# Performance work log

Hardware: AMD Instinct MI355X
Metric: run time of the kernel (lower is better)

## Reference

```python
import jax, jax.numpy as jnp
import numpy as np

B, S, T, H, E, V = 64, 128, 64, 512, 256, 10000


def setup_inputs() -> dict:
    key = jax.random.key(0)
    ks = jax.random.split(key, 16)
    w = 0.05
    return {
        "trg": jax.random.randint(ks[0], (B, T), 0, V),
        "encoder_hidden": jax.random.normal(ks[1], (B, S, 2 * H), jnp.float32),
        "src_lengths": jax.random.randint(ks[2], (B,), 1, S + 1),
        "h0": jax.random.normal(ks[3], (B, H), jnp.float32),
        "c0": jax.random.normal(ks[4], (B, H), jnp.float32),
        "emb_table": jax.random.normal(ks[5], (V, E), jnp.float32) * w,
        "Wkey": jax.random.normal(ks[6], (2 * H, H), jnp.float32) * w,      # attention.key_layer
        "Wquery": jax.random.normal(ks[7], (H, H), jnp.float32) * w,        # attention.query_layer
        "we": jax.random.normal(ks[8], (H,), jnp.float32) * w,              # attention.energy_layer
        "W_ih": jax.random.normal(ks[9], (4 * H, E + 2 * H), jnp.float32) * w,
        "W_hh": jax.random.normal(ks[10], (4 * H, H), jnp.float32) * w,
        "b_ih": jnp.zeros((4 * H,), jnp.float32),
        "b_hh": jnp.zeros((4 * H,), jnp.float32),
        "Wpre": jax.random.normal(ks[11], (3 * H + E, H), jnp.float32) * w,  # pre_output_layer (no bias)
        "Wgen": jax.random.normal(ks[12], (H, V), jnp.float32) * w,          # generator / softmax head
    }


def reference(trg, encoder_hidden, src_lengths, h0, c0, emb_table, Wkey, Wquery,
              we, W_ih, W_hh, b_ih, b_hh, Wpre, Wgen):
    # Teacher-forced unroll (teacher_forcing=True branch); dropout in eval mode.
    s = encoder_hidden.shape[1]
    proj_key = encoder_hidden @ Wkey                            # [B,S,H]
    mask = jnp.arange(s)[None, :] < src_lengths[:, None]        # [B,S]
    embs = emb_table[trg]                                       # [B,T,E]

    def step(carry, emb_t):
        h, c = carry                                            # [B,H] each
        q = h @ Wquery                                          # query = last-layer hidden
        e = jnp.einsum('bsh,h->bs', jnp.tanh(q[:, None, :] + proj_key), we)
        a = jax.nn.softmax(jnp.where(mask, e, -1e9), axis=-1)   # masked attention
        ctx = jnp.einsum('bs,bsd->bd', a, encoder_hidden)       # [B,2H]
        x = jnp.concatenate([emb_t, ctx], axis=-1)              # rnn_input
        g = x @ W_ih.T + h @ W_hh.T + b_ih + b_hh
        i_g, f_g, g_g, o_g = jnp.split(g, 4, axis=-1)           # torch LSTM gate order
        c_new = jax.nn.sigmoid(f_g) * c + jax.nn.sigmoid(i_g) * jnp.tanh(g_g)
        h_new = jax.nn.sigmoid(o_g) * jnp.tanh(c_new)
        pre = jnp.concatenate([emb_t, h_new, ctx], axis=-1) @ Wpre
        logp = jax.nn.log_softmax(pre @ Wgen, axis=-1)          # [B,V]
        return (h_new, c_new), logp

    (hf, cf), out = jax.lax.scan(step, (h0, c0), jnp.swapaxes(embs, 0, 1))
    return jnp.transpose(out, (1, 2, 0)), hf, cf                # out: [B,V,T]
```

## Files before the change

### kernel.cpp

```cpp
#include <hip/hip_runtime.h>

#define B 64
#define S 128
#define T 64
#define H 512
#define E 256
#define V 10000
#define H2 1024
#define G4 2048
#define KX 1536
#define KP 1792
#define VP 10112
#define NROW 4096

typedef unsigned short u16;
typedef __attribute__((ext_vector_type(8))) short bf16x8;
typedef __attribute__((ext_vector_type(4))) short bf16x4;
typedef __attribute__((ext_vector_type(4))) float floatx4;

__device__ inline float b2f(u16 h){
  union { unsigned int u; float f; } v; v.u = ((unsigned int)h) << 16; return v.f;
}
__device__ inline u16 f2b(float f){
  union { unsigned int u; float f; } v; v.f = f;
  unsigned int r = v.u + 0x7FFFu + ((v.u >> 16) & 1u);
  return (u16)(r >> 16);
}
__device__ __forceinline__ float rcpf(float x){ return __builtin_amdgcn_rcpf(x); }
__device__ inline float sigf(float x){ return rcpf(1.f + __expf(-x)); }
__device__ inline float tanh_fast(float x){ float e=__expf(2.f*x); return 1.f - 2.f*rcpf(e+1.f); }

__device__ __forceinline__ void st_wt_u32(u16* p, unsigned v){
  asm volatile("global_store_dword %0, %1, off sc0 sc1" :: "v"(p), "v"(v) : "memory");
}
__device__ __forceinline__ void st_wt_u16(u16* p, unsigned v){
  asm volatile("global_store_short %0, %1, off sc0 sc1" :: "v"(p), "v"(v) : "memory");
}
__device__ __forceinline__ unsigned ld_if(unsigned* p){
  unsigned v;
  asm volatile("global_load_dword %0, %1, off sc0 sc1\ns_waitcnt vmcnt(0)" : "=v"(v) : "v"(p) : "memory");
  return v;
}
__device__ __forceinline__ void st_if(unsigned* p, unsigned v){
  asm volatile("global_store_dword %0, %1, off sc0 sc1\ns_waitcnt vmcnt(0)" :: "v"(p), "v"(v) : "memory");
}

#define BAR_WORDS (128*64)

__global__ void k_cast(const float* __restrict__ src, u16* __restrict__ dst, int n){
  int i = blockIdx.x*256 + threadIdx.x;
  if (i < n) dst[i] = f2b(src[i]);
}
__global__ void k_tct(const float* __restrict__ src, u16* __restrict__ dst, int R, int C){
  __shared__ float tile[64][65];
  int c0 = blockIdx.x*64, r0 = blockIdx.y*64;
  int tid = threadIdx.x;
  #pragma unroll
  for (int i=0;i<16;i++){
    int flat = i*256 + tid;
    int rr = flat >> 6, cc = flat & 63;
    int c = c0 + cc;
    tile[rr][cc] = (c < C) ? src[(size_t)(r0+rr)*C + c] : 0.f;
  }
  __syncthreads();
  #pragma unroll
  for (int i=0;i<16;i++){
    int flat = i*256 + tid;
    int cc = flat >> 6, rr = flat & 63;
    dst[(size_t)(c0+cc)*R + r0 + rr] = f2b(tile[rr][cc]);
  }
}
__global__ void k_encT(const float* __restrict__ enc, u16* __restrict__ o){
  __shared__ float tile[64][65];
  int d0 = blockIdx.x*64, s0 = blockIdx.y*64, b = blockIdx.z;
  int tid = threadIdx.x;
  #pragma unroll
  for (int i=0;i<16;i++){
    int flat = i*256 + tid;
    int sl = flat >> 6, dl = flat & 63;
    tile[sl][dl] = enc[((size_t)(b*S) + s0+sl)*H2 + d0+dl];
  }
  __syncthreads();
  #pragma unroll
  for (int i=0;i<16;i++){
    int flat = i*256 + tid;
    int dl = flat >> 6, sl = flat & 63;
    o[((size_t)b*H2 + d0+dl)*S + s0+sl] = f2b(tile[sl][dl]);
  }
}
__global__ void k_wch(const float* __restrict__ wih, const float* __restrict__ whh, u16* __restrict__ o){
  int i = blockIdx.x*256 + threadIdx.x;
  if (i < G4*KX){
    int gp = i / KX, k = i % KX;
    int j = gp >> 2, gate = gp & 3, g = gate*H + j;
    float v = (k < H2) ? wih[(size_t)g*(E+H2) + E + k] : whh[(size_t)g*H + (k - H2)];
    o[i] = f2b(v);
  }
}
__global__ void k_wihe(const float* __restrict__ wih, u16* __restrict__ o){
  int i = blockIdx.x*256 + threadIdx.x;
  if (i < G4*E){
    int gp = i / E, e = i % E;
    int j = gp >> 2, gate = gp & 3, g = gate*H + j;
    o[i] = f2b(wih[(size_t)g*(E+H2) + e]);
  }
}
__global__ void k_bias(const float* __restrict__ bi, const float* __restrict__ bh, float* __restrict__ o){
  int i = blockIdx.x*256 + threadIdx.x;
  if (i < G4){
    int j = i >> 2, gate = i & 3, g = gate*H + j;
    o[i] = bi[g] + bh[g];
  }
}
__global__ void k_emb(const int* __restrict__ trg, const float* __restrict__ emb, u16* __restrict__ catp){
  int i = blockIdx.x*256 + threadIdx.x;
  if (i < NROW*E){
    int row = i >> 8, e = i & 255;
    int tok = trg[row];
    catp[(size_t)row*KP + e] = f2b(emb[(size_t)tok*E + e]);
  }
}
__global__ void k_init(const float* __restrict__ h0, u16* __restrict__ xgs){
  int i = blockIdx.x*256 + threadIdx.x;
  if (i < B*H){
    int b = i >> 9, j = i & 511;
    xgs[(size_t)b*KX + H2 + j] = f2b(h0[i]);
  }
}
__global__ void k_zero(unsigned* bar){
  int i = blockIdx.x*256 + threadIdx.x;
  if (i < BAR_WORDS) bar[i] = 0u;
}
__global__ void k_lse(const float* __restrict__ sep, float* __restrict__ lse){
  int r = blockIdx.x*256 + threadIdx.x;
  if (r < NROW){
    float s = 0.f;
    for (int i=0;i<79;i++) s += sep[(size_t)r*80 + i];
    lse[r] = logf(s);
  }
}

template<int TN, int EPI>
__global__ __launch_bounds__(256) void gemm_bf16(
    const u16* __restrict__ A, int lda,
    const u16* __restrict__ BT, int ldb,
    int K,
    u16* outb, int ldc,
    float* sep,
    float* outp, const float* lse)
{
  constexpr int NSUB = TN/16;
  constexpr int NB = TN/64;
  __shared__ u16 sA[64*32];
  __shared__ u16 sB[TN*32];
  __shared__ float Cx[(EPI==3) ? 128*65 : 1];
  __shared__ float lseb[(EPI==3)?64:1];

  const int tid = threadIdx.x;
  const int lane = tid & 63;
  const int wv = tid >> 6;
  const int row0 = blockIdx.x * 64;
  const int n0 = blockIdx.y * TN;

  floatx4 acc[NSUB];
  #pragma unroll
  for (int s=0;s<NSUB;s++) acc[s] = (floatx4){0.f,0.f,0.f,0.f};

  const int ar = tid >> 2;
  const int ch = tid & 3;
  const int swz = (ar >> 1) & 3;
  const int px = ((lane & 15) >> 1) & 3;

  const u16* gA = A + (size_t)(row0+ar)*lda + ch*8;
  bf16x8 pa = *(const bf16x8*)gA;
  bf16x8 pb[NB];
  #pragma unroll
  for (int i=0;i<NB;i++) pb[i] = *(const bf16x8*)(BT + (size_t)(n0+i*64+ar)*ldb + ch*8);

  for (int k0 = 0; k0 < K; k0 += 32){
    __syncthreads();
    *(bf16x8*)&sA[ar*32 + ((ch ^ swz)*8)] = pa;
    #pragma unroll
    for (int i=0;i<NB;i++)
      *(bf16x8*)&sB[(i*64+ar)*32 + ((ch ^ swz)*8)] = pb[i];
    __syncthreads();
    if (k0 + 32 < K){
      pa = *(const bf16x8*)(gA + k0 + 32);
      #pragma unroll
      for (int i=0;i<NB;i++) pb[i] = *(const bf16x8*)(BT + (size_t)(n0+i*64+ar)*ldb + k0+32 + ch*8);
    }
    bf16x8 af = *(const bf16x8*)&sA[(16*wv + (lane&15))*32 + (((lane>>4) ^ px)*8)];
    #pragma unroll
    for (int s=0;s<NSUB;s++){
      bf16x8 bfv = *(const bf16x8*)&sB[(16*s + (lane&15))*32 + (((lane>>4) ^ px)*8)];
      acc[s] = __builtin_amdgcn_mfma_f32_16x16x32_bf16(af, bfv, acc[s], 0, 0, 0);
    }
  }

  if constexpr (EPI == 0 || EPI == 4){
    #pragma unroll
    for (int s=0;s<NSUB;s++)
      #pragma unroll
      for (int r=0;r<4;r++){
        int row = row0 + 16*wv + ((lane>>4)<<2) + r;
        int col = n0 + 16*s + (lane&15);
        if (EPI == 4) row = ((row & 63) << 6) | (row >> 6);
        outb[(size_t)row*ldc + col] = f2b(acc[s][r]);
      }
  }
  if constexpr (EPI == 2){
    float sr[4] = {0.f,0.f,0.f,0.f};
    #pragma unroll
    for (int s=0;s<NSUB;s++){
      int col = n0 + 16*s + (lane&15);
      if (col < V){
        #pragma unroll
        for (int r=0;r<4;r++) sr[r] += __expf(acc[s][r]);
      }
    }
    #pragma unroll
    for (int r=0;r<4;r++){
      float v = sr[r];
      v += __shfl_xor(v,1); v += __shfl_xor(v,2); v += __shfl_xor(v,4); v += __shfl_xor(v,8);
      sr[r] = v;
    }
    if ((lane&15)==0){
      #pragma unroll
      for (int r=0;r<4;r++){
        int row = row0 + 16*wv + ((lane>>4)<<2) + r;
        sep[(size_t)row*80 + blockIdx.y] = sr[r];
      }
    }
  }
  if constexpr (EPI == 3){
    #pragma unroll
    for (int s=0;s<NSUB;s++)
      #pragma unroll
      for (int r=0;r<4;r++){
        int rl = 16*wv + ((lane>>4)<<2) + r;
        int cl = 16*s + (lane&15);
        Cx[cl*65 + rl] = acc[s][r];
      }
    if (tid < 64) lseb[tid] = lse[row0 + tid];
    __syncthreads();
    int b = blockIdx.x;
    for (int idx = tid; idx < TN*16; idx += 256){
      int vl = idx >> 4, q4 = idx & 15;
      int v = n0 + vl;
      if (v < V){
        floatx4 o;
        o[0] = Cx[vl*65 + q4*4+0] - lseb[q4*4+0];
        o[1] = Cx[vl*65 + q4*4+1] - lseb[q4*4+1];
        o[2] = Cx[vl*65 + q4*4+2] - lseb[q4*4+2];
        o[3] = Cx[vl*65 + q4*4+3] - lseb[q4*4+3];
        *(floatx4*)&outp[((size_t)b*V + v)*T + q4*4] = o;
      }
    }
  }
}

__device__ __forceinline__ void wait_flags(unsigned* base, unsigned g){
  if (threadIdx.x < 64){
    unsigned* p = base + (unsigned)threadIdx.x*64;
    if (ld_if(p) < g){
      int it = 0;
      do { asm volatile("s_sleep 8":::); } while (ld_if(p) < g && ++it < 1000000);
    }
  }
  __syncthreads();
}

__global__ __launch_bounds__(512) void decoder_loop(
    u16* __restrict__ xgs, const float* __restrict__ c0f, float* __restrict__ outp,
    const u16* __restrict__ pk, const u16* __restrict__ encbT,
    const float* __restrict__ we, const int* __restrict__ lens,
    const u16* __restrict__ wqT, u16* __restrict__ cph,
    const u16* __restrict__ wch, const u16* __restrict__ gembt,
    const float* __restrict__ bias, unsigned* __restrict__ bar)
{
  __shared__ char pool[140288];

  const int tid = threadIdx.x, lane = tid & 63, wv = tid >> 6;
  const int blk = blockIdx.x;
  const int xcd = blk & 7, slot = blk >> 3;
  unsigned* flag_ctx = bar;
  unsigned* flag_h   = bar + 64*64;

  if (slot < 8){
    u16*   hsb  = (u16*)pool;
    float* qw   = (float*)(pool + 1024);
    float* wel  = (float*)(pool + 3072);
    float* ep   = (float*)(pool + 5120);
    float* ev   = (float*)(pool + 7168);
    u16*   alb  = (u16*)(pool + 7680);
    float* ctxf = (float*)(pool + 8192);

    const int b = xcd*8 + slot;
    const int lenb = lens[b];
    const int nks = (lenb + 31) >> 5;
    wel[tid] = we[tid];
    __syncthreads();

    for (int t=0; t<T; t++){
      wait_flags(flag_h, (unsigned)t);
      u16* xgt = xgs + (size_t)t*B*KX;
      hsb[tid] = xgt[b*KX + H2 + tid];
      __syncthreads();
      {
        floatx4 accq[4];
        #pragma unroll
        for (int s=0;s<4;s++) accq[s] = (floatx4){0.f,0.f,0.f,0.f};
        const int kc = (lane>>4)*8;
        #pragma unroll 4
        for (int ks=0; ks<16; ks++){
          bf16x8 af = *(const bf16x8*)&hsb[ks*32 + kc];
          #pragma unroll
          for (int s=0;s<4;s++){
            const u16* bp = wqT + (size_t)(wv*64 + s*16 + (lane&15))*H + ks*32 + kc;
            accq[s] = __builtin_amdgcn_mfma_f32_16x16x32_bf16(af, *(const bf16x8*)bp, accq[s], 0, 0, 0);
          }
        }
        if (lane < 16){
          #pragma unroll
          for (int s=0;s<4;s++) qw[wv*64 + s*16 + lane] = accq[s][0];
        }
      }
      __syncthreads();
      {
        int s = tid >> 2, part = tid & 3;
        float a0 = 0.f;
        if (s < lenb){
          const u16* pr = pk + (size_t)(b*S + s)*H;
          #pragma unroll 4
          for (int m=0;m<16;m++){
            int k0 = part*8 + m*32;
            bf16x8 p8 = *(const bf16x8*)(pr + k0);
            floatx4 qa = *(const floatx4*)&qw[k0];
            floatx4 qb = *(const floatx4*)&qw[k0+4];
            floatx4 wa = *(const floatx4*)&wel[k0];
            floatx4 wb = *(const floatx4*)&wel[k0+4];
            #pragma unroll
            for (int i=0;i<4;i++){
              a0 += tanh_fast(qa[i] + b2f((u16)p8[i]))   * wa[i];
              a0 += tanh_fast(qb[i] + b2f((u16)p8[i+4])) * wb[i];
            }
          }
        }
        ep[tid] = a0;
      }
      __syncthreads();
      if (wv == 0){
        int s0 = lane, s1 = lane + 64;
        float e0 = ep[s0*4]+ep[s0*4+1]+ep[s0*4+2]+ep[s0*4+3];
        float e1 = ep[s1*4]+ep[s1*4+1]+ep[s1*4+2]+ep[s1*4+3];
        bool m0 = s0 < lenb, m1 = s1 < lenb;
        float mx = fmaxf(m0 ? e0 : -1e30f, m1 ? e1 : -1e30f);
        #pragma unroll
        for (int o=32;o>=1;o>>=1) mx = fmaxf(mx, __shfl_xor(mx,o));
        float p0 = m0 ? __expf(e0-mx) : 0.f;
        float p1 = m1 ? __expf(e1-mx) : 0.f;
        float sm = p0 + p1;
        #pragma unroll
        for (int o=32;o>=1;o>>=1) sm += __shfl_xor(sm,o);
        float sinv = rcpf(sm);
        alb[s0] = f2b(p0*sinv);
        alb[s1] = f2b(p1*sinv);
      }
      __syncthreads();
      {
        floatx4 accc[8];
        #pragma unroll
        for (int s=0;s<8;s++) accc[s] = (floatx4){0.f,0.f,0.f,0.f};
        const int kc = (lane>>4)*8;
        for (int ks=0; ks<nks; ks++){
          bf16x8 af = *(const bf16x8*)&alb[ks*32 + kc];
          #pragma unroll
          for (int s8=0;s8<8;s8++){
            const u16* bp = encbT + ((size_t)b*H2 + wv*128 + s8*16 + (lane&15))*S + ks*32 + kc;
            accc[s8] = __builtin_amdgcn_mfma_f32_16x16x32_bf16(af, *(const bf16x8*)bp, accc[s8], 0, 0, 0);
          }
        }
        if (lane < 16){
          #pragma unroll
          for (int s8=0;s8<8;s8++) ctxf[wv*128 + s8*16 + lane] = accc[s8][0];
        }
      }
      __syncthreads();
      {
        int d = tid*2;
        unsigned pack = ((unsigned)f2b(ctxf[d+1]) << 16) | (unsigned)f2b(ctxf[d]);
        st_wt_u32(xgt + (size_t)b*KX + d, pack);
        *(unsigned*)&cph[(size_t)(b*T + t)*KP + E + H + d] = pack;
      }
      asm volatile("s_waitcnt vmcnt(0)" ::: "memory");
      __syncthreads();
      if (tid == 0) st_if(flag_ctx + (unsigned)b*64, (unsigned)(t+1));
      __syncthreads();
    }
  } else {
    u16*   sB  = (u16*)pool;
    u16*   sA0 = (u16*)(pool + 98304);
    u16*   sA1 = (u16*)(pool + 114688);
    float* Cx  = (float*)(pool + 131072);

    const int g = slot - 8;
    const int gid = xcd*8 + g;
    const int n0 = xcd*256 + g*32;
    const int kh = wv >> 2, wr = wv & 3;
    const int rs0 = tid >> 4, gs = tid & 15;
    const int rowa = 16*wr + (lane & 15);
    const int pb_ = tid >> 3, jl = tid & 7;
    const int jglob = n0/4 + jl;
    float creg = c0f[pb_*H + jglob];
    floatx4 bias4 = *(const floatx4*)(bias + n0 + jl*4);

    for (int u = tid; u < 32*192; u += 512){
      int row = u / 192, cl = u % 192;
      int kk = cl >> 4, c = cl & 15;
      *(bf16x8*)&sB[row*1536 + kk*128 + ((c ^ (row&7))*8)] =
          *(const bf16x8*)(wch + (size_t)(n0+row)*KX + kk*128 + c*8);
    }
    __syncthreads();

    for (int t=0; t<T; t++){
      const u16* xgt = xgs + (size_t)t*B*KX;
      u16* xgn = xgs + (size_t)(t+1)*B*KX;
      bf16x4 g4 = *(const bf16x4*)(gembt + (size_t)(t*B + pb_)*G4 + n0 + jl*4);

      floatx4 gacc[2];
      gacc[0] = (floatx4){0.f,0.f,0.f,0.f};
      gacc[1] = (floatx4){0.f,0.f,0.f,0.f};

      {
        bf16x8 a0 = *(const bf16x8*)(xgt + (size_t)rs0*KX + 8*128 + gs*8);
        bf16x8 a1 = *(const bf16x8*)(xgt + (size_t)(rs0+32)*KX + 8*128 + gs*8);
        for (int kk=8; kk<12; kk++){
          u16* sAc = (kk & 1) ? sA1 : sA0;
          *(bf16x8*)&sAc[rs0*128 + ((gs ^ (rs0&7))*8)] = a0;
          *(bf16x8*)&sAc[(rs0+32)*128 + ((gs ^ (rs0&7))*8)] = a1;
          __syncthreads();
          if (kk < 11){
            int ko = (kk+1)*128;
            a0 = *(const bf16x8*)(xgt + (size_t)rs0*KX + ko + gs*8);
            a1 = *(const bf16x8*)(xgt + (size_t)(rs0+32)*KX + ko + gs*8);
          }
          #pragma unroll
          for (int ks=0; ks<2; ks++){
            int gq = kh*8 + ks*4 + (lane>>4);
            bf16x8 af = *(const bf16x8*)&sAc[rowa*128 + ((gq ^ (rowa&7))*8)];
            #pragma unroll
            for (int s=0;s<2;s++){
              int rowb = 16*s + (lane & 15);
              bf16x8 bfv = *(const bf16x8*)&sB[rowb*1536 + kk*128 + ((gq ^ (rowb&7))*8)];
              gacc[s] = __builtin_amdgcn_mfma_f32_16x16x32_bf16(af, bfv, gacc[s], 0, 0, 0);
            }
          }
          __syncthreads();
        }
      }
      wait_flags(flag_ctx, (unsigned)(t+1));
      {
        bf16x8 a0 = *(const bf16x8*)(xgt + (size_t)rs0*KX + gs*8);
        bf16x8 a1 = *(const bf16x8*)(xgt + (size_t)(rs0+32)*KX + gs*8);
        for (int kk=0; kk<8; kk++){
          u16* sAc = (kk & 1) ? sA1 : sA0;
          *(bf16x8*)&sAc[rs0*128 + ((gs ^ (rs0&7))*8)] = a0;
          *(bf16x8*)&sAc[(rs0+32)*128 + ((gs ^ (rs0&7))*8)] = a1;
          __syncthreads();
          if (kk < 7){
            int ko = (kk+1)*128;
            a0 = *(const bf16x8*)(xgt + (size_t)rs0*KX + ko + gs*8);
            a1 = *(const bf16x8*)(xgt + (size_t)(rs0+32)*KX + ko + gs*8);
          }
          #pragma unroll
          for (int ks=0; ks<2; ks++){
            int gq = kh*8 + ks*4 + (lane>>4);
            bf16x8 af = *(const bf16x8*)&sAc[rowa*128 + ((gq ^ (rowa&7))*8)];
            #pragma unroll
            for (int s=0;s<2;s++){
              int rowb = 16*s + (lane & 15);
              bf16x8 bfv = *(const bf16x8*)&sB[rowb*1536 + kk*128 + ((gq ^ (rowb&7))*8)];
              gacc[s] = __builtin_amdgcn_mfma_f32_16x16x32_bf16(af, bfv, gacc[s], 0, 0, 0);
            }
          }
          __syncthreads();
        }
      }
      {
        int r0 = 16*wr + ((lane>>4)<<2);
        if (kh == 1){
          #pragma unroll
          for (int s=0;s<2;s++)
            #pragma unroll
            for (int r=0;r<4;r++) Cx[(r0+r)*36 + 16*s + (lane&15)] = gacc[s][r];
        }
      }
      __syncthreads();
      {
        int r0 = 16*wr + ((lane>>4)<<2);
        if (kh == 0){
          #pragma unroll
          for (int s=0;s<2;s++)
            #pragma unroll
            for (int r=0;r<4;r++) Cx[(r0+r)*36 + 16*s + (lane&15)] += gacc[s][r];
        }
      }
      __syncthreads();
      {
        float gi = Cx[pb_*36 + jl*4+0] + b2f((u16)g4[0]) + bias4[0];
        float gf = Cx[pb_*36 + jl*4+1] + b2f((u16)g4[1]) + bias4[1];
        float gg = Cx[pb_*36 + jl*4+2] + b2f((u16)g4[2]) + bias4[2];
        float go = Cx[pb_*36 + jl*4+3] + b2f((u16)g4[3]) + bias4[3];
        float cn = sigf(gf)*creg + sigf(gi)*tanh_fast(gg);
        float hn = sigf(go)*tanh_fast(cn);
        creg = cn;
        u16 hb = f2b(hn);
        st_wt_u16(xgn + (size_t)pb_*KX + H2 + jglob, (unsigned)hb);
        cph[(size_t)(pb_*T + t)*KP + E + jglob] = hb;
        if (t == T-1){
          outp[(size_t)B*V*T + pb_*H + jglob] = hn;
          outp[(size_t)B*V*T + B*H + pb_*H + jglob] = cn;
        }
      }
      asm volatile("s_waitcnt vmcnt(0)" ::: "memory");
      __syncthreads();
      if (tid == 0) st_if(flag_h + (unsigned)gid*64, (unsigned)(t+1));
      __syncthreads();
    }
  }
}

static inline int cdiv(int a, int b){ return (a + b - 1) / b; }

extern "C" void kernel_launch(void* const* d_in, const int* in_sizes, int n_in,
                              void* d_out, int out_size, void* d_ws, size_t ws_size,
                              hipStream_t stream)
{
  (void)in_sizes; (void)n_in; (void)out_size; (void)ws_size;
  const int*   trg  = (const int*)d_in[0];
  const float* enc  = (const float*)d_in[1];
  const int*   lens = (const int*)d_in[2];
  const float* h0   = (const float*)d_in[3];
  const float* c0   = (const float*)d_in[4];
  const float* embt = (const float*)d_in[5];
  const float* wkey = (const float*)d_in[6];
  const float* wqry = (const float*)d_in[7];
  const float* we   = (const float*)d_in[8];
  const float* wih  = (const float*)d_in[9];
  const float* whh  = (const float*)d_in[10];
  const float* bi   = (const float*)d_in[11];
  const float* bh   = (const float*)d_in[12];
  const float* wpre = (const float*)d_in[13];
  const float* wgen = (const float*)d_in[14];
  float* out = (float*)d_out;

  char* p = (char*)d_ws;
  auto carve = [&](size_t bytes)->char*{ char* r = p; p += (bytes + 255) & ~(size_t)255; return r; };
  u16*   encb  = (u16*)  carve((size_t)B*S*H2*2);
  u16*   encbT = (u16*)  carve((size_t)B*H2*S*2);
  u16*   pkb   = (u16*)  carve((size_t)B*S*H*2);
  u16*   catp  = (u16*)  carve((size_t)NROW*KP*2);
  u16*   gembb = (u16*)  carve((size_t)NROW*G4*2);
  u16*   preb  = (u16*)  carve((size_t)NROW*H*2);
  u16*   wgt   = (u16*)  carve((size_t)VP*H*2);
  u16*   wch   = (u16*)  carve((size_t)G4*KX*2);
  u16*   wihe  = (u16*)  carve((size_t)G4*E*2);
  u16*   wkeyT = (u16*)  carve((size_t)H*H2*2);
  u16*   wqT   = (u16*)  carve((size_t)H*H*2);
  u16*   wpreT = (u16*)  carve((size_t)H*KP*2);
  u16*   xgs   = (u16*)  carve((size_t)(T+1)*B*KX*2);
  float* biasp = (float*)carve((size_t)G4*4);
  float* sep   = (float*)carve((size_t)NROW*80*4);
  float* lse   = (float*)carve((size_t)NROW*4);
  unsigned* bar = (unsigned*)carve(BAR_WORDS*4);

  k_cast<<<cdiv(B*S*H2,256),256,0,stream>>>(enc, encb, B*S*H2);
  k_encT<<<dim3(H2/64, S/64, B),256,0,stream>>>(enc, encbT);
  k_tct<<<dim3(H/64, H/64),256,0,stream>>>(wqry, wqT, H, H);
  k_tct<<<dim3(H/64, H2/64),256,0,stream>>>(wkey, wkeyT, H2, H);
  k_tct<<<dim3(H/64, KP/64),256,0,stream>>>(wpre, wpreT, KP, H);
  k_tct<<<dim3(VP/64, H/64),256,0,stream>>>(wgen, wgt, H, V);
  k_wch<<<cdiv(G4*KX,256),256,0,stream>>>(wih, whh, wch);
  k_wihe<<<cdiv(G4*E,256),256,0,stream>>>(wih, wihe);
  k_bias<<<cdiv(G4,256),256,0,stream>>>(bi, bh, biasp);
  k_emb<<<cdiv(NROW*E,256),256,0,stream>>>(trg, embt, catp);
  k_init<<<cdiv(B*H,256),256,0,stream>>>(h0, xgs);
  k_zero<<<cdiv(BAR_WORDS,256),256,0,stream>>>(bar);

  gemm_bf16<64,0><<<dim3(B*S/64, H/64),256,0,stream>>>(
      encb, H2, wkeyT, H2, H2, pkb, H, nullptr, nullptr, nullptr);
  gemm_bf16<64,4><<<dim3(NROW/64, G4/64),256,0,stream>>>(
      catp, KP, wihe, E, E, gembb, G4, nullptr, nullptr, nullptr);

  decoder_loop<<<128,512,0,stream>>>(xgs, c0, out, pkb, encbT, we, lens,
                                     wqT, catp, wch, gembb, biasp, bar);

  gemm_bf16<64,0><<<dim3(NROW/64, H/64),256,0,stream>>>(
      catp, KP, wpreT, KP, KP, preb, H, nullptr, nullptr, nullptr);

  gemm_bf16<128,2><<<dim3(NROW/64, VP/128),256,0,stream>>>(
      preb, H, wgt, H, H, nullptr, 0, sep, nullptr, nullptr);
  k_lse<<<cdiv(NROW,256),256,0,stream>>>(sep, lse);
  gemm_bf16<128,3><<<dim3(NROW/64, VP/128),256,0,stream>>>(
      preb, H, wgt, H, H, nullptr, 0, nullptr, out, lse);
}
```

Measured before the change: 2.516 ms.

## Repartition LSTM gate blocks by batch group to localize cross-block synchronization

Gate blocks now each own 8 batch rows and 64 hidden units (all four gates) instead of all 64 batch rows for 32 gate columns. Each block then waits on only 8 flags, the attention blocks for its batch group and the hidden-state producers it depends on, instead of all 64. Gate weights are no longer held in LDS; they are streamed from global memory with register prefetch, which cuts LDS use and removes the K-split reduction and the double-buffered A staging. Spin-wait sleep is also shortened. The cost is more weight traffic from global/L2 on every step, and MFMA tiles are half wasted because only 8 of 16 rows are used.

```diff
diff --git a/kernel.cpp b/kernel.cpp
--- a/kernel.cpp
+++ b/kernel.cpp
@@ -259,12 +259,12 @@
   }
 }
 
-__device__ __forceinline__ void wait_flags(unsigned* base, unsigned g){
-  if (threadIdx.x < 64){
-    unsigned* p = base + (unsigned)threadIdx.x*64;
+__device__ __forceinline__ void wait8(unsigned* bar, int base, int stride, unsigned g){
+  if (threadIdx.x < 8){
+    unsigned* p = bar + (unsigned)(base + (int)threadIdx.x*stride)*64;
     if (ld_if(p) < g){
       int it = 0;
-      do { asm volatile("s_sleep 8":::); } while (ld_if(p) < g && ++it < 1000000);
+      do { asm volatile("s_sleep 2":::); } while (ld_if(p) < g && ++it < 2000000);
     }
   }
   __syncthreads();
@@ -278,31 +278,29 @@
     const u16* __restrict__ wch, const u16* __restrict__ gembt,
     const float* __restrict__ bias, unsigned* __restrict__ bar)
 {
-  __shared__ char pool[140288];
+  __shared__ char pool[61440];
 
   const int tid = threadIdx.x, lane = tid & 63, wv = tid >> 6;
   const int blk = blockIdx.x;
   const int xcd = blk & 7, slot = blk >> 3;
-  unsigned* flag_ctx = bar;
-  unsigned* flag_h   = bar + 64*64;
 
   if (slot < 8){
     u16*   hsb  = (u16*)pool;
     float* qw   = (float*)(pool + 1024);
     float* wel  = (float*)(pool + 3072);
     float* ep   = (float*)(pool + 5120);
-    float* ev   = (float*)(pool + 7168);
     u16*   alb  = (u16*)(pool + 7680);
     float* ctxf = (float*)(pool + 8192);
 
     const int b = xcd*8 + slot;
+    const int x = xcd;
     const int lenb = lens[b];
     const int nks = (lenb + 31) >> 5;
     wel[tid] = we[tid];
     __syncthreads();
 
     for (int t=0; t<T; t++){
-      wait_flags(flag_h, (unsigned)t);
+      wait8(bar, 64 + x, 8, (unsigned)t);
       u16* xgt = xgs + (size_t)t*B*KX;
       hsb[tid] = xgt[b*KX + H2 + tid];
       __syncthreads();
@@ -394,137 +392,95 @@
       }
       asm volatile("s_waitcnt vmcnt(0)" ::: "memory");
       __syncthreads();
-      if (tid == 0) st_if(flag_ctx + (unsigned)b*64, (unsigned)(t+1));
+      if (tid == 0) st_if(bar + (unsigned)b*64, (unsigned)(t+1));
       __syncthreads();
     }
   } else {
-    u16*   sB  = (u16*)pool;
-    u16*   sA0 = (u16*)(pool + 98304);
-    u16*   sA1 = (u16*)(pool + 114688);
-    float* Cx  = (float*)(pool + 131072);
-
-    const int g = slot - 8;
-    const int gid = xcd*8 + g;
-    const int n0 = xcd*256 + g*32;
-    const int kh = wv >> 2, wr = wv & 3;
-    const int rs0 = tid >> 4, gs = tid & 15;
-    const int rowa = 16*wr + (lane & 15);
-    const int pb_ = tid >> 3, jl = tid & 7;
-    const int jglob = n0/4 + jl;
-    float creg = c0f[pb_*H + jglob];
-    floatx4 bias4 = *(const floatx4*)(bias + n0 + jl*4);
-
-    for (int u = tid; u < 32*192; u += 512){
-      int row = u / 192, cl = u % 192;
-      int kk = cl >> 4, c = cl & 15;
-      *(bf16x8*)&sB[row*1536 + kk*128 + ((c ^ (row&7))*8)] =
-          *(const bf16x8*)(wch + (size_t)(n0+row)*KX + kk*128 + c*8);
-    }
-    __syncthreads();
+    u16*   xA = (u16*)pool;
+    float* Cg = (float*)(pool + 49152);
+
+    const int g = xcd;
+    const int x = slot - 8;
+    const int b0g = x*8;
+    const int jl = tid & 63, bloc = tid >> 6;
+    const int jglob = g*64 + jl;
+    float creg = c0f[(b0g + bloc)*H + jglob];
+    floatx4 bias4 = *(const floatx4*)(bias + g*256 + jl*4);
+    const u16* bpB = wch + (size_t)(g*256 + wv*32 + (lane&15))*KX + (lane>>4)*8;
 
     for (int t=0; t<T; t++){
       const u16* xgt = xgs + (size_t)t*B*KX;
       u16* xgn = xgs + (size_t)(t+1)*B*KX;
-      bf16x4 g4 = *(const bf16x4*)(gembt + (size_t)(t*B + pb_)*G4 + n0 + jl*4);
-
-      floatx4 gacc[2];
-      gacc[0] = (floatx4){0.f,0.f,0.f,0.f};
-      gacc[1] = (floatx4){0.f,0.f,0.f,0.f};
-
-      {
-        bf16x8 a0 = *(const bf16x8*)(xgt + (size_t)rs0*KX + 8*128 + gs*8);
-        bf16x8 a1 = *(const bf16x8*)(xgt + (size_t)(rs0+32)*KX + 8*128 + gs*8);
-        for (int kk=8; kk<12; kk++){
-          u16* sAc = (kk & 1) ? sA1 : sA0;
-          *(bf16x8*)&sAc[rs0*128 + ((gs ^ (rs0&7))*8)] = a0;
-          *(bf16x8*)&sAc[(rs0+32)*128 + ((gs ^ (rs0&7))*8)] = a1;
-          __syncthreads();
-          if (kk < 11){
-            int ko = (kk+1)*128;
-            a0 = *(const bf16x8*)(xgt + (size_t)rs0*KX + ko + gs*8);
-            a1 = *(const bf16x8*)(xgt + (size_t)(rs0+32)*KX + ko + gs*8);
+
+      wait8(bar, 64 + x, 8, (unsigned)t);
+      {
+        int row = tid >> 6, cl = tid & 63;
+        int kk = 8 + (cl >> 4), c = cl & 15;
+        *(bf16x8*)&xA[kk*2048 + row*128 + ((c ^ row)*8)] =
+            *(const bf16x8*)(xgt + (size_t)(b0g+row)*KX + kk*128 + c*8);
+      }
+      bf16x4 g4 = *(const bf16x4*)(gembt + (size_t)(t*B + b0g + bloc)*G4 + g*256 + jl*4);
+
+      wait8(bar, 8*x, 1, (unsigned)(t+1));
+      #pragma unroll
+      for (int i=0;i<2;i++){
+        int u = tid + i*512;
+        int row = u >> 7, cl = u & 127;
+        int kk = cl >> 4, c = cl & 15;
+        *(bf16x8*)&xA[kk*2048 + row*128 + ((c ^ row)*8)] =
+            *(const bf16x8*)(xgt + (size_t)(b0g+row)*KX + kk*128 + c*8);
+      }
+      __syncthreads();
+
+      floatx4 a0 = (floatx4){0.f,0.f,0.f,0.f};
+      floatx4 a1 = (floatx4){0.f,0.f,0.f,0.f};
+      {
+        const int rowa = lane & 15;
+        bf16x8 bc0 = *(const bf16x8*)(bpB);
+        bf16x8 bc1 = *(const bf16x8*)(bpB + (size_t)16*KX);
+        for (int kk=0; kk<48; kk++){
+          bf16x8 bn0, bn1;
+          if (kk < 47){
+            bn0 = *(const bf16x8*)(bpB + (kk+1)*32);
+            bn1 = *(const bf16x8*)(bpB + (size_t)16*KX + (kk+1)*32);
           }
+          int gq = (kk & 3)*4 + (lane>>4);
+          bf16x8 af = *(const bf16x8*)&xA[(kk>>2)*2048 + rowa*128 + ((gq ^ (rowa&7))*8)];
+          a0 = __builtin_amdgcn_mfma_f32_16x16x32_bf16(af, bc0, a0, 0, 0, 0);
+          a1 = __builtin_amdgcn_mfma_f32_16x16x32_bf16(af, bc1, a1, 0, 0, 0);
+          bc0 = bn0; bc1 = bn1;
+        }
+      }
+      {
+        int rbase = (lane>>4)*4;
+        if (rbase < 8){
           #pragma unroll
-          for (int ks=0; ks<2; ks++){
-            int gq = kh*8 + ks*4 + (lane>>4);
-            bf16x8 af = *(const bf16x8*)&sAc[rowa*128 + ((gq ^ (rowa&7))*8)];
-            #pragma unroll
-            for (int s=0;s<2;s++){
-              int rowb = 16*s + (lane & 15);
-              bf16x8 bfv = *(const bf16x8*)&sB[rowb*1536 + kk*128 + ((gq ^ (rowb&7))*8)];
-              gacc[s] = __builtin_amdgcn_mfma_f32_16x16x32_bf16(af, bfv, gacc[s], 0, 0, 0);
-            }
+          for (int r=0;r<4 && rbase+r<8;r++){
+            Cg[(rbase+r)*264 + wv*32 + (lane&15)]      = a0[r];
+            Cg[(rbase+r)*264 + wv*32 + 16 + (lane&15)] = a1[r];
           }
-          __syncthreads();
-        }
-      }
-      wait_flags(flag_ctx, (unsigned)(t+1));
-      {
-        bf16x8 a0 = *(const bf16x8*)(xgt + (size_t)rs0*KX + gs*8);
-        bf16x8 a1 = *(const bf16x8*)(xgt + (size_t)(rs0+32)*KX + gs*8);
-        for (int kk=0; kk<8; kk++){
-          u16* sAc = (kk & 1) ? sA1 : sA0;
-          *(bf16x8*)&sAc[rs0*128 + ((gs ^ (rs0&7))*8)] = a0;
-          *(bf16x8*)&sAc[(rs0+32)*128 + ((gs ^ (rs0&7))*8)] = a1;
-          __syncthreads();
-          if (kk < 7){
-            int ko = (kk+1)*128;
-            a0 = *(const bf16x8*)(xgt + (size_t)rs0*KX + ko + gs*8);
-            a1 = *(const bf16x8*)(xgt + (size_t)(rs0+32)*KX + ko + gs*8);
-          }
-          #pragma unroll
-          for (int ks=0; ks<2; ks++){
-            int gq = kh*8 + ks*4 + (lane>>4);
-            bf16x8 af = *(const bf16x8*)&sAc[rowa*128 + ((gq ^ (rowa&7))*8)];
-            #pragma unroll
-            for (int s=0;s<2;s++){
-              int rowb = 16*s + (lane & 15);
-              bf16x8 bfv = *(const bf16x8*)&sB[rowb*1536 + kk*128 + ((gq ^ (rowb&7))*8)];
-              gacc[s] = __builtin_amdgcn_mfma_f32_16x16x32_bf16(af, bfv, gacc[s], 0, 0, 0);
-            }
-          }
-          __syncthreads();
-        }
-      }
-      {
-        int r0 = 16*wr + ((lane>>4)<<2);
-        if (kh == 1){
-          #pragma unroll
-          for (int s=0;s<2;s++)
-            #pragma unroll
-            for (int r=0;r<4;r++) Cx[(r0+r)*36 + 16*s + (lane&15)] = gacc[s][r];
-        }
-      }
-      __syncthreads();
-      {
-        int r0 = 16*wr + ((lane>>4)<<2);
-        if (kh == 0){
-          #pragma unroll
-          for (int s=0;s<2;s++)
-            #pragma unroll
-            for (int r=0;r<4;r++) Cx[(r0+r)*36 + 16*s + (lane&15)] += gacc[s][r];
-        }
-      }
-      __syncthreads();
-      {
-        float gi = Cx[pb_*36 + jl*4+0] + b2f((u16)g4[0]) + bias4[0];
-        float gf = Cx[pb_*36 + jl*4+1] + b2f((u16)g4[1]) + bias4[1];
-        float gg = Cx[pb_*36 + jl*4+2] + b2f((u16)g4[2]) + bias4[2];
-        float go = Cx[pb_*36 + jl*4+3] + b2f((u16)g4[3]) + bias4[3];
+        }
+      }
+      __syncthreads();
+      {
+        float gi = Cg[bloc*264 + jl*4+0] + b2f((u16)g4[0]) + bias4[0];
+        float gf = Cg[bloc*264 + jl*4+1] + b2f((u16)g4[1]) + bias4[1];
+        float gg = Cg[bloc*264 + jl*4+2] + b2f((u16)g4[2]) + bias4[2];
+        float go = Cg[bloc*264 + jl*4+3] + b2f((u16)g4[3]) + bias4[3];
         float cn = sigf(gf)*creg + sigf(gi)*tanh_fast(gg);
         float hn = sigf(go)*tanh_fast(cn);
         creg = cn;
         u16 hb = f2b(hn);
-        st_wt_u16(xgn + (size_t)pb_*KX + H2 + jglob, (unsigned)hb);
-        cph[(size_t)(pb_*T + t)*KP + E + jglob] = hb;
+        st_wt_u16(xgn + (size_t)(b0g+bloc)*KX + H2 + jglob, (unsigned)hb);
+        cph[(size_t)((b0g+bloc)*T + t)*KP + E + jglob] = hb;
         if (t == T-1){
-          outp[(size_t)B*V*T + pb_*H + jglob] = hn;
-          outp[(size_t)B*V*T + B*H + pb_*H + jglob] = cn;
+          outp[(size_t)B*V*T + (b0g+bloc)*H + jglob] = hn;
+          outp[(size_t)B*V*T + B*H + (b0g+bloc)*H + jglob] = cn;
         }
       }
       asm volatile("s_waitcnt vmcnt(0)" ::: "memory");
       __syncthreads();
-      if (tid == 0) st_if(flag_h + (unsigned)gid*64, (unsigned)(t+1));
+      if (tid == 0) st_if(bar + (unsigned)(64 + g*8 + x)*64, (unsigned)(t+1));
       __syncthreads();
     }
   }
```

After: 3.794 ms. 50.8% more time.

## Load gate-GEMM A fragments directly from global into registers, drop LDS staging

Applied to the files above, without the earlier changes.

The gate GEMM in the LSTM blocks no longer stages activation tiles through double-buffered shared memory with per-chunk barriers. Each wave now loads its 24 A fragments straight from global memory into registers and splits K by wave half instead of interleaving. Waves covering the embedding/h part prefetch before waiting on the context flag. This removes about 24 block barriers per step and cuts LDS usage, at the cost of higher register pressure and uncoalesced, redundant global loads. The spin-wait sleep is also shortened to poll more often.

```diff
diff --git a/kernel.cpp b/kernel.cpp
--- a/kernel.cpp
+++ b/kernel.cpp
@@ -264,7 +264,7 @@
     unsigned* p = base + (unsigned)threadIdx.x*64;
     if (ld_if(p) < g){
       int it = 0;
-      do { asm volatile("s_sleep 8":::); } while (ld_if(p) < g && ++it < 1000000);
+      do { asm volatile("s_sleep 4":::); } while (ld_if(p) < g && ++it < 1500000);
     }
   }
   __syncthreads();
@@ -278,7 +278,7 @@
     const u16* __restrict__ wch, const u16* __restrict__ gembt,
     const float* __restrict__ bias, unsigned* __restrict__ bar)
 {
-  __shared__ char pool[140288];
+  __shared__ char pool[107520];
 
   const int tid = threadIdx.x, lane = tid & 63, wv = tid >> 6;
   const int blk = blockIdx.x;
@@ -291,7 +291,6 @@
     float* qw   = (float*)(pool + 1024);
     float* wel  = (float*)(pool + 3072);
     float* ep   = (float*)(pool + 5120);
-    float* ev   = (float*)(pool + 7168);
     u16*   alb  = (u16*)(pool + 7680);
     float* ctxf = (float*)(pool + 8192);
 
@@ -399,20 +398,21 @@
     }
   } else {
     u16*   sB  = (u16*)pool;
-    u16*   sA0 = (u16*)(pool + 98304);
-    u16*   sA1 = (u16*)(pool + 114688);
-    float* Cx  = (float*)(pool + 131072);
+    float* Cx  = (float*)(pool + 98304);
 
     const int g = slot - 8;
     const int gid = xcd*8 + g;
     const int n0 = xcd*256 + g*32;
     const int kh = wv >> 2, wr = wv & 3;
-    const int rs0 = tid >> 4, gs = tid & 15;
-    const int rowa = 16*wr + (lane & 15);
     const int pb_ = tid >> 3, jl = tid & 7;
     const int jglob = n0/4 + jl;
     float creg = c0f[pb_*H + jglob];
     floatx4 bias4 = *(const floatx4*)(bias + n0 + jl*4);
+
+    const int arow = 16*wr + (lane & 15);
+    const int kq8  = (lane >> 4) * 8;
+    const int rowb0 = (lane & 15);
+    const int rowb1 = 16 + (lane & 15);
 
     for (int u = tid; u < 32*192; u += 512){
       int row = u / 192, cl = u % 192;
@@ -427,65 +427,35 @@
       u16* xgn = xgs + (size_t)(t+1)*B*KX;
       bf16x4 g4 = *(const bf16x4*)(gembt + (size_t)(t*B + pb_)*G4 + n0 + jl*4);
 
+      const u16* aBase = xgt + (size_t)arow*KX + kh*768 + kq8;
+      bf16x8 fa[24];
+      if (kh == 1){
+        #pragma unroll
+        for (int c=8;c<24;c++) fa[c] = *(const bf16x8*)(aBase + c*32);
+      }
+      wait_flags(flag_ctx, (unsigned)(t+1));
+      if (kh == 1){
+        #pragma unroll
+        for (int c=0;c<8;c++) fa[c] = *(const bf16x8*)(aBase + c*32);
+      } else {
+        #pragma unroll
+        for (int c=0;c<24;c++) fa[c] = *(const bf16x8*)(aBase + c*32);
+      }
+
       floatx4 gacc[2];
       gacc[0] = (floatx4){0.f,0.f,0.f,0.f};
       gacc[1] = (floatx4){0.f,0.f,0.f,0.f};
-
-      {
-        bf16x8 a0 = *(const bf16x8*)(xgt + (size_t)rs0*KX + 8*128 + gs*8);
-        bf16x8 a1 = *(const bf16x8*)(xgt + (size_t)(rs0+32)*KX + 8*128 + gs*8);
-        for (int kk=8; kk<12; kk++){
-          u16* sAc = (kk & 1) ? sA1 : sA0;
-          *(bf16x8*)&sAc[rs0*128 + ((gs ^ (rs0&7))*8)] = a0;
-          *(bf16x8*)&sAc[(rs0+32)*128 + ((gs ^ (rs0&7))*8)] = a1;
-          __syncthreads();
-          if (kk < 11){
-            int ko = (kk+1)*128;
-            a0 = *(const bf16x8*)(xgt + (size_t)rs0*KX + ko + gs*8);
-            a1 = *(const bf16x8*)(xgt + (size_t)(rs0+32)*KX + ko + gs*8);
-          }
-          #pragma unroll
-          for (int ks=0; ks<2; ks++){
-            int gq = kh*8 + ks*4 + (lane>>4);
-            bf16x8 af = *(const bf16x8*)&sAc[rowa*128 + ((gq ^ (rowa&7))*8)];
-            #pragma unroll
-            for (int s=0;s<2;s++){
-              int rowb = 16*s + (lane & 15);
-              bf16x8 bfv = *(const bf16x8*)&sB[rowb*1536 + kk*128 + ((gq ^ (rowb&7))*8)];
-              gacc[s] = __builtin_amdgcn_mfma_f32_16x16x32_bf16(af, bfv, gacc[s], 0, 0, 0);
-            }
-          }
-          __syncthreads();
-        }
-      }
-      wait_flags(flag_ctx, (unsigned)(t+1));
-      {
-        bf16x8 a0 = *(const bf16x8*)(xgt + (size_t)rs0*KX + gs*8);
-        bf16x8 a1 = *(const bf16x8*)(xgt + (size_t)(rs0+32)*KX + gs*8);
-        for (int kk=0; kk<8; kk++){
-          u16* sAc = (kk & 1) ? sA1 : sA0;
-          *(bf16x8*)&sAc[rs0*128 + ((gs ^ (rs0&7))*8)] = a0;
-          *(bf16x8*)&sAc[(rs0+32)*128 + ((gs ^ (rs0&7))*8)] = a1;
-          __syncthreads();
-          if (kk < 7){
-            int ko = (kk+1)*128;
-            a0 = *(const bf16x8*)(xgt + (size_t)rs0*KX + ko + gs*8);
-            a1 = *(const bf16x8*)(xgt + (size_t)(rs0+32)*KX + ko + gs*8);
-          }
-          #pragma unroll
-          for (int ks=0; ks<2; ks++){
-            int gq = kh*8 + ks*4 + (lane>>4);
-            bf16x8 af = *(const bf16x8*)&sAc[rowa*128 + ((gq ^ (rowa&7))*8)];
-            #pragma unroll
-            for (int s=0;s<2;s++){
-              int rowb = 16*s + (lane & 15);
-              bf16x8 bfv = *(const bf16x8*)&sB[rowb*1536 + kk*128 + ((gq ^ (rowb&7))*8)];
-              gacc[s] = __builtin_amdgcn_mfma_f32_16x16x32_bf16(af, bfv, gacc[s], 0, 0, 0);
-            }
-          }
-          __syncthreads();
-        }
-      }
+      #pragma unroll
+      for (int c=0;c<24;c++){
+        int kcb = kh*768 + c*32;
+        int kk = kcb >> 7;
+        int gq = ((kcb & 127) >> 3) + (lane >> 4);
+        bf16x8 b0 = *(const bf16x8*)&sB[rowb0*1536 + kk*128 + ((gq ^ (rowb0&7))*8)];
+        bf16x8 b1 = *(const bf16x8*)&sB[rowb1*1536 + kk*128 + ((gq ^ (rowb1&7))*8)];
+        gacc[0] = __builtin_amdgcn_mfma_f32_16x16x32_bf16(fa[c], b0, gacc[0], 0, 0, 0);
+        gacc[1] = __builtin_amdgcn_mfma_f32_16x16x32_bf16(fa[c], b1, gacc[1], 0, 0, 0);
+      }
+
       {
         int r0 = 16*wr + ((lane>>4)<<2);
         if (kh == 1){
```

Measured after the change: 2.541 ms. No clear change (+1.0%).
